# Performance work log

Measured on AMD Instinct MI355X. Metric: run time of the kernel, lower is better.

Reference implementation:

```python
import jax, jax.numpy as jnp
import numpy as np
from jax import lax

COMMITMENT_COST = 0.25

def setup_inputs() -> dict:
    key = jax.random.key(0)
    k1, k2, k3, k4 = jax.random.split(key, 4)
    B, C, H, W, K = 32, 128, 32, 32, 8192
    return {
        "x": jax.random.normal(k1, (B, C, H, W), dtype=jnp.float32),
        "W_lin": jax.random.normal(k2, (C, C), dtype=jnp.float32) * (1.0 / np.sqrt(C)),
        "b_lin": jax.random.normal(k3, (C,), dtype=jnp.float32) * 0.01,
        "emb": jax.random.normal(k4, (K, C), dtype=jnp.float32),
    }

def reference(x, W_lin, b_lin, emb):
    B, C, H, W = x.shape
    K = emb.shape[0]
    # BCHW -> BHWC, then linear projection
    inp = jnp.transpose(x, (0, 2, 3, 1))          # [B,H,W,C]
    inp = inp @ W_lin.T + b_lin                   # nn.Linear
    flat = inp.reshape(-1, C)                     # [N,C], N=B*H*W
    # squared L2 distances to codebook: ||z||^2 + ||e||^2 - 2 z.e
    d = (jnp.sum(flat**2, axis=1, keepdims=True)
         + jnp.sum(emb**2, axis=1)
         - 2.0 * flat @ emb.T)                    # [N,K]
    idx = jnp.argmin(d, axis=1)                   # [N]
    quantized = emb[idx].reshape(inp.shape)       # gather == onehot @ emb
    e_latent = jnp.mean((lax.stop_gradient(quantized) - inp) ** 2)
    q_latent = jnp.mean((quantized - lax.stop_gradient(inp)) ** 2)
    loss = q_latent + COMMITMENT_COST * e_latent
    # straight-through estimator
    quantized_st = inp + lax.stop_gradient(quantized - inp)
    # perplexity from code usage histogram (== mean of one-hot encodings)
    counts = jnp.zeros((K,), dtype=flat.dtype).at[idx].add(1.0)
    avg_probs = counts / flat.shape[0]
    perplexity = jnp.exp(-jnp.sum(avg_probs * jnp.log(avg_probs + 1e-10)))
    out = jnp.transpose(quantized_st, (0, 3, 1, 2))  # back to BCHW
    return (loss, out, perplexity, idx[:, None])
```

## Files before the change

### kernel.cpp

```cpp
#include <hip/hip_runtime.h>
#include <hip/hip_bf16.h>
#include <float.h>

#define NPIX   32768
#define CDIM   128
#define KCB    8192
#define EPS_STOP 0.30f
#define TAUF   0.012f
#define RCAP   8192
#define RCAPA  2048

typedef _Float16 f16x8 __attribute__((ext_vector_type(8)));
typedef float    f32x16 __attribute__((ext_vector_type(16)));

#define WS_EMBFH   0
#define WS_E2      2359296
#define WS_ZWS     2392064
#define WS_CAND    19169280
#define WS_IDX     20217856
#define WS_RLISTA  20348928
#define WS_RLISTB  20381696
#define WS_SCAND   20512768
#define WS_SCANI   21037056
#define WS_COUNTS  21299200
#define WS_LOSS    21331968
#define WS_RCNTA   21331972
#define WS_RCNTB   21331976
#define WS_ZERO_OFF 21299200
#define WS_ZERO_LEN 32780

#define OUT_OFF_OUT  1
#define OUT_OFF_PERP 4194305
#define OUT_OFF_IDX  4194306

__device__ __forceinline__ void ins6(float f, float v[6]) {
    float a = fmaxf(v[0], f); v[0] = fminf(v[0], f);
    float b = fmaxf(v[1], a); v[1] = fminf(v[1], a);
    a = fmaxf(v[2], b); v[2] = fminf(v[2], b);
    b = fmaxf(v[3], a); v[3] = fminf(v[3], a);
    a = fmaxf(v[4], b); v[4] = fminf(v[4], b);
    v[5] = fminf(v[5], a);
}

__global__ __launch_bounds__(256) void k_e2(const float* __restrict__ emb, float* __restrict__ e2) {
    int t = threadIdx.x;
    int wv = t >> 6, l = t & 63;
    int k = blockIdx.x * 4 + wv;
    const float2 v = *(const float2*)&emb[(size_t)k * 128 + l * 2];
    float s = v.x * v.x + v.y * v.y;
    #pragma unroll
    for (int o = 32; o; o >>= 1) s += __shfl_down(s, o, 64);
    if (l == 0) e2[k] = s;
}

__global__ __launch_bounds__(256) void k_prep(const float* __restrict__ emb, const float* __restrict__ e2,
                                              _Float16* __restrict__ embFh) {
    int tid = blockIdx.x * 256 + threadIdx.x;
    int m = tid / 18, r = tid % 18;
    int s = r >> 1, h = r & 1;
    f16x8 hv;
    #pragma unroll
    for (int j = 0; j < 8; ++j) hv[j] = (_Float16)0.0f;
    if (s < 8) {
        int c0 = s * 16 + h * 8;
        const float4 a = *(const float4*)&emb[(size_t)m * 128 + c0];
        const float4 b = *(const float4*)&emb[(size_t)m * 128 + c0 + 4];
        float vals[8] = {a.x, a.y, a.z, a.w, b.x, b.y, b.z, b.w};
        #pragma unroll
        for (int j = 0; j < 8; ++j) hv[j] = (_Float16)(-2.0f * vals[j]);
    } else if (h == 0) {
        float v = e2[m] + 512.0f;
        _Float16 eh = (_Float16)v;
        hv[0] = eh;
        hv[1] = (_Float16)(v - (float)eh);
    }
    size_t base = (((size_t)(m >> 5) * 9 + s) * 64 + (m & 31) + h * 32) * 8;
    *(f16x8*)&embFh[base] = hv;
}

__global__ __launch_bounds__(256, 2) void k_main(
    const float* __restrict__ x, const float* __restrict__ Wl, const float* __restrict__ bl,
    const _Float16* __restrict__ embFh,
    float* __restrict__ zws, float4* __restrict__ cand)
{
    __shared__ __align__(16) float As[64 * 132];
    __shared__ __align__(16) float Xs[64 * 66];
    __shared__ float z2p[256];

    const int t  = threadIdx.x;
    const int n0 = blockIdx.x * 64;
    const int b  = n0 >> 10;
    const int hw0 = n0 & 1023;

    {
        const int p = t & 63, ig = t >> 6;
        float accz[32];
        const float4* bl4 = (const float4*)(bl + ig * 32);
        #pragma unroll
        for (int q = 0; q < 8; ++q) {
            float4 v = bl4[q];
            accz[4*q+0] = v.x; accz[4*q+1] = v.y; accz[4*q+2] = v.z; accz[4*q+3] = v.w;
        }
        for (int hf = 0; hf < 2; ++hf) {
            __syncthreads();
            for (int r = 0; r < 16; ++r) {
                int lin = r * 256 + t;
                int cc = lin >> 6, pp = lin & 63;
                Xs[cc * 66 + pp] = x[(size_t)(b * 128 + hf * 64 + cc) * 1024 + hw0 + pp];
            }
            __syncthreads();
            for (int cc4 = 0; cc4 < 16; ++cc4) {
                float xv0 = Xs[(cc4*4+0) * 66 + p];
                float xv1 = Xs[(cc4*4+1) * 66 + p];
                float xv2 = Xs[(cc4*4+2) * 66 + p];
                float xv3 = Xs[(cc4*4+3) * 66 + p];
                #pragma unroll
                for (int ii = 0; ii < 32; ++ii) {
                    const float4 w4 = *(const float4*)&Wl[(size_t)(ig*32+ii) * 128 + hf*64 + cc4*4];
                    float a = accz[ii];
                    a = fmaf(w4.x, xv0, a);
                    a = fmaf(w4.y, xv1, a);
                    a = fmaf(w4.z, xv2, a);
                    a = fmaf(w4.w, xv3, a);
                    accz[ii] = a;
                }
            }
        }
        float ssq = 0.f;
        float4* ao = (float4*)&As[p * 132 + ig * 32];
        float4* zo = (float4*)(zws + (size_t)(n0 + p) * 128 + ig * 32);
        #pragma unroll
        for (int q = 0; q < 8; ++q) {
            float4 v = make_float4(accz[4*q+0], accz[4*q+1], accz[4*q+2], accz[4*q+3]);
            ao[q] = v;
            zo[q] = v;
            ssq = fmaf(v.x, v.x, fmaf(v.y, v.y, fmaf(v.z, v.z, fmaf(v.w, v.w, ssq))));
        }
        z2p[p * 4 + ig] = ssq;
    }
    __syncthreads();

    const int l = t & 63, w = t >> 6;
    const int half = l >> 5, pcol = l & 31;
    f16x8 B0[9], B1[9];
    #pragma unroll
    for (int nt = 0; nt < 2; ++nt) {
        int p = nt * 32 + pcol;
        #pragma unroll
        for (int s = 0; s < 8; ++s) {
            const float* zp = &As[p * 132 + s * 16 + half * 8];
            float4 v0 = *(const float4*)zp;
            float4 v1 = *(const float4*)(zp + 4);
            float vals[8] = {v0.x, v0.y, v0.z, v0.w, v1.x, v1.y, v1.z, v1.w};
            f16x8 hh;
            #pragma unroll
            for (int j2 = 0; j2 < 8; ++j2) hh[j2] = (_Float16)vals[j2];
            if (nt == 0) B0[s] = hh; else B1[s] = hh;
        }
    }
    {
        f16x8 b8;
        #pragma unroll
        for (int j2 = 0; j2 < 8; ++j2) b8[j2] = (_Float16)0.0f;
        if (half == 0) { b8[0] = (_Float16)1.0f; b8[1] = (_Float16)1.0f; }
        B0[8] = b8; B1[8] = b8;
    }

    auto tree16 = [](const f32x16& v) -> float {
        float a = fminf(fminf(v[0], v[1]), fminf(v[2], v[3]));
        float bb = fminf(fminf(v[4], v[5]), fminf(v[6], v[7]));
        float c = fminf(fminf(v[8], v[9]), fminf(v[10], v[11]));
        float d = fminf(fminf(v[12], v[13]), fminf(v[14], v[15]));
        return fminf(fminf(a, bb), fminf(c, d));
    };

    float gv[6] = {3e38f, 3e38f, 3e38f, 3e38f, 3e38f, 3e38f};
    float hv[6] = {3e38f, 3e38f, 3e38f, 3e38f, 3e38f, 3e38f};
    const f16x8* Ahp = (const f16x8*)embFh;
    f16x8 aE[9], aO[9];
    {
        const f16x8* P = Ahp + (size_t)w * 576 + l;
        #pragma unroll
        for (int s = 0; s < 9; ++s) aE[s] = P[s * 64];
    }
    {
        const f16x8* P = Ahp + (size_t)(w + 4) * 576 + l;
        #pragma unroll
        for (int s = 0; s < 9; ++s) aO[s] = P[s * 64];
    }
    uint32_t idv = (uint32_t)((w << 1) | half);

    for (int g = w; g < 256; g += 8) {
        {
            f32x16 c00 = {}, c01 = {}, c10 = {}, c11 = {};
            #pragma unroll
            for (int s = 0; s < 9; ++s) {
                if (s & 1) {
                    c01 = __builtin_amdgcn_mfma_f32_32x32x16_f16(aE[s], B0[s], c01, 0, 0, 0);
                    c11 = __builtin_amdgcn_mfma_f32_32x32x16_f16(aE[s], B1[s], c11, 0, 0, 0);
                } else {
                    c00 = __builtin_amdgcn_mfma_f32_32x32x16_f16(aE[s], B0[s], c00, 0, 0, 0);
                    c10 = __builtin_amdgcn_mfma_f32_32x32x16_f16(aE[s], B1[s], c10, 0, 0, 0);
                }
            }
            f32x16 s0, s1;
            #pragma unroll
            for (int r = 0; r < 16; ++r) { s0[r] = c00[r] + c01[r]; s1[r] = c10[r] + c11[r]; }
            float m0 = tree16(s0), m1 = tree16(s1);
            ins6(__uint_as_float((__float_as_uint(m0) & 0xFFFFFE00u) | idv), gv);
            ins6(__uint_as_float((__float_as_uint(m1) & 0xFFFFFE00u) | idv), hv);
        }
        {
            int gn = (g + 8 < 256) ? (g + 8) : w;
            const f16x8* P = Ahp + (size_t)gn * 576 + l;
            #pragma unroll
            for (int s = 0; s < 9; ++s) aE[s] = P[s * 64];
        }
        {
            f32x16 c00 = {}, c01 = {}, c10 = {}, c11 = {};
            #pragma unroll
            for (int s = 0; s < 9; ++s) {
                if (s & 1) {
                    c01 = __builtin_amdgcn_mfma_f32_32x32x16_f16(aO[s], B0[s], c01, 0, 0, 0);
                    c11 = __builtin_amdgcn_mfma_f32_32x32x16_f16(aO[s], B1[s], c11, 0, 0, 0);
                } else {
                    c00 = __builtin_amdgcn_mfma_f32_32x32x16_f16(aO[s], B0[s], c00, 0, 0, 0);
                    c10 = __builtin_amdgcn_mfma_f32_32x32x16_f16(aO[s], B1[s], c10, 0, 0, 0);
                }
            }
            f32x16 s0, s1;
            #pragma unroll
            for (int r = 0; r < 16; ++r) { s0[r] = c00[r] + c01[r]; s1[r] = c10[r] + c11[r]; }
            float m0 = tree16(s0), m1 = tree16(s1);
            uint32_t ido = idv + 8u;
            ins6(__uint_as_float((__float_as_uint(m0) & 0xFFFFFE00u) | ido), gv);
            ins6(__uint_as_float((__float_as_uint(m1) & 0xFFFFFE00u) | ido), hv);
        }
        {
            int gn = (g + 12 < 256) ? (g + 12) : w;
            const f16x8* P = Ahp + (size_t)gn * 576 + l;
            #pragma unroll
            for (int s = 0; s < 9; ++s) aO[s] = P[s * 64];
        }
        idv += 16u;
    }

    __syncthreads();
    float* Ms = Xs;
    const int slot = (w << 1) | half;
    #pragma unroll
    for (int q = 0; q < 6; ++q) {
        Ms[(pcol * 8 + slot) * 6 + q] = gv[q];
        Ms[((32 + pcol) * 8 + slot) * 6 + q] = hv[q];
    }
    __syncthreads();
    if (t < 64) {
        float v6[6] = {3e38f, 3e38f, 3e38f, 3e38f, 3e38f, 3e38f};
        #pragma unroll
        for (int s = 0; s < 48; ++s) ins6(Ms[t * 48 + s], v6);
        float z2 = z2p[t*4+0] + z2p[t*4+1] + z2p[t*4+2] + z2p[t*4+3];
        cand[(size_t)(n0 + t) * 2 + 0] = make_float4(v6[0], v6[1], v6[2], v6[3]);
        cand[(size_t)(n0 + t) * 2 + 1] = make_float4(v6[4], v6[5], z2, 0.f);
    }
}

__global__ __launch_bounds__(256) void k_rec(
    const float* __restrict__ zws, const float* __restrict__ emb,
    const float4* __restrict__ cand, int* __restrict__ idxws,
    float* __restrict__ out_idxf, float* __restrict__ losssum,
    int* __restrict__ rlistA, int* __restrict__ rcntA,
    int* __restrict__ rlistB, int* __restrict__ rcntB)
{
    __shared__ float lred[16];
    const int t = threadIdx.x;
    const int pl = t >> 4, j = t & 15;
    const int n = blockIdx.x * 16 + pl;

    const float4 za = *(const float4*)&zws[(size_t)n * 128 + j * 8];
    const float4 zb = *(const float4*)&zws[(size_t)n * 128 + j * 8 + 4];
    const float4 c0 = cand[(size_t)n * 2 + 0];
    const float4 c1 = cand[(size_t)n * 2 + 1];
    const float pv[6] = {c0.x, c0.y, c0.z, c0.w, c1.x, c1.y};
    const float pbase = c1.z - 512.0f;

    float d1 = 3e38f, d2 = 3e38f; int i1 = 0x7fffffff, i2 = 0x7fffffff;
    bool safe = false;
    float lastgmin = 0.f;
    for (int q = 0; q < 6; ++q) {
        uint32_t bits = __float_as_uint(pv[q]);
        float gmin = __uint_as_float(bits & 0xFFFFFE00u);
        lastgmin = gmin;
        if (gmin >= d1 - pbase + EPS_STOP) { safe = true; break; }
        const int mbase = (int)((bits >> 1) & 255u) * 32 + (int)((bits & 1u) << 2);
        #pragma unroll
        for (int c = 0; c < 16; ++c) {
            int m = mbase + (c & 3) + 8 * (c >> 2);
            const float4 ea = *(const float4*)&emb[(size_t)m * 128 + j * 8];
            const float4 eb = *(const float4*)&emb[(size_t)m * 128 + j * 8 + 4];
            float da0 = za.x - ea.x, da1 = za.y - ea.y, da2 = za.z - ea.z, da3 = za.w - ea.w;
            float db0 = zb.x - eb.x, db1 = zb.y - eb.y, db2 = zb.z - eb.z, db3 = zb.w - eb.w;
            float s = da0*da0; s = fmaf(da1, da1, s); s = fmaf(da2, da2, s); s = fmaf(da3, da3, s);
            s = fmaf(db0, db0, s); s = fmaf(db1, db1, s); s = fmaf(db2, db2, s); s = fmaf(db3, db3, s);
            s += __shfl_xor(s, 1, 16);
            s += __shfl_xor(s, 2, 16);
            s += __shfl_xor(s, 4, 16);
            s += __shfl_xor(s, 8, 16);
            if (s < d1 || (s == d1 && m < i1)) { d2 = d1; i2 = i1; d1 = s; i1 = m; }
            else if (s < d2) { d2 = s; i2 = m; }
        }
    }
    if (!safe && lastgmin >= d1 - pbase + EPS_STOP) safe = true;

    if (j == 0) {
        idxws[n] = i1;
        out_idxf[n] = (float)i1;
        if (!safe) {
            int s = atomicAdd(rcntA, 1);
            if (s < RCAPA) rlistA[s] = n;
        } else if ((d2 - d1) < TAUF) {
            int s = atomicAdd(rcntB, 1);
            if (s < RCAP) { int4 v4 = make_int4(n, i1, i2, 0); ((int4*)rlistB)[s] = v4; }
        }
        lred[pl] = d1;
    }
    __syncthreads();
    if (t == 0) {
        float ls = 0.f;
        #pragma unroll
        for (int q = 0; q < 16; ++q) ls += lred[q];
        atomicAdd(losssum, ls);
    }
}

__global__ __launch_bounds__(256) void k_scanp(
    const float* __restrict__ zws, const float* __restrict__ emb,
    const int* __restrict__ rcntA, const int* __restrict__ rlistA,
    double* __restrict__ scand, int* __restrict__ scani)
{
    int cnt = *rcntA; if (cnt > RCAPA) cnt = RCAPA;
    const int t = threadIdx.x;
    const int chunk = blockIdx.x & 31;
    const int gi = t >> 4, j = t & 15;
    __shared__ double sd[16];
    __shared__ int si[16];
    for (int e = blockIdx.x >> 5; e < cnt; e += 64) {
        const int n = rlistA[e];
        const float4 za = *(const float4*)&zws[(size_t)n * 128 + j * 8];
        const float4 zb = *(const float4*)&zws[(size_t)n * 128 + j * 8 + 4];
        double best = 1e300; int bi = 0x7fffffff;
        const int kbase = chunk * 256 + gi * 16;
        for (int c = 0; c < 16; ++c) {
            const int m = kbase + c;
            const float4 ea = *(const float4*)&emb[(size_t)m * 128 + j * 8];
            const float4 eb = *(const float4*)&emb[(size_t)m * 128 + j * 8 + 4];
            double s = 0.0, d;
            d = (double)za.x - (double)ea.x; s += d * d;
            d = (double)za.y - (double)ea.y; s += d * d;
            d = (double)za.z - (double)ea.z; s += d * d;
            d = (double)za.w - (double)ea.w; s += d * d;
            d = (double)zb.x - (double)eb.x; s += d * d;
            d = (double)zb.y - (double)eb.y; s += d * d;
            d = (double)zb.z - (double)eb.z; s += d * d;
            d = (double)zb.w - (double)eb.w; s += d * d;
            s += __shfl_xor(s, 1, 16);
            s += __shfl_xor(s, 2, 16);
            s += __shfl_xor(s, 4, 16);
            s += __shfl_xor(s, 8, 16);
            if (s < best) { best = s; bi = m; }
        }
        __syncthreads();
        if (j == 0) { sd[gi] = best; si[gi] = bi; }
        __syncthreads();
        if (t == 0) {
            double b = sd[0]; int ib = si[0];
            #pragma unroll
            for (int q = 1; q < 16; ++q)
                if (sd[q] < b || (sd[q] == b && si[q] < ib)) { b = sd[q]; ib = si[q]; }
            scand[e * 32 + chunk] = b;
            scani[e * 32 + chunk] = ib;
        }
    }
}

__global__ __launch_bounds__(64) void k_mergeA(
    const int* __restrict__ rcntA, const int* __restrict__ rlistA,
    const double* __restrict__ scand, const int* __restrict__ scani,
    int* __restrict__ idxws, float* __restrict__ out_idxf)
{
    int cnt = *rcntA; if (cnt > RCAPA) cnt = RCAPA;
    const int t = threadIdx.x;
    for (int e = blockIdx.x; e < cnt; e += gridDim.x) {
        double b = 1e300; int ib = 0x7fffffff;
        if (t < 32) { b = scand[e * 32 + t]; ib = scani[e * 32 + t]; }
        #pragma unroll
        for (int o = 16; o; o >>= 1) {
            double ob = __shfl_down(b, o, 64);
            int oi = __shfl_down(ib, o, 64);
            if (ob < b || (ob == b && oi < ib)) { b = ob; ib = oi; }
        }
        if (t == 0) { int n = rlistA[e]; idxws[n] = ib; out_idxf[n] = (float)ib; }
    }
}

__global__ __launch_bounds__(128) void k_pairB(
    const float* __restrict__ x, const float* __restrict__ Wl, const float* __restrict__ bl,
    const float* __restrict__ emb, const int* __restrict__ rcntB, const int* __restrict__ rlistB,
    int* __restrict__ idxws, float* __restrict__ out_idxf)
{
    __shared__ double xs[128];
    __shared__ double red[128];
    int cnt = *rcntB; if (cnt > RCAP) cnt = RCAP;
    const int t = threadIdx.x;
    for (int e = blockIdx.x; e < cnt; e += gridDim.x) {
        const int4 v = ((const int4*)rlistB)[e];
        const int n = v.x, c1 = v.y, c2 = v.z;
        const int b = n >> 10, hw = n & 1023;
        __syncthreads();
        xs[t] = (double)x[(size_t)(b * 128 + t) * 1024 + hw];
        __syncthreads();
        double z = (double)bl[t];
        for (int c = 0; c < 128; ++c) z = fma((double)Wl[(size_t)t * 128 + c], xs[c], z);
        double d1v, d2v;
        double da = z - (double)emb[(size_t)c1 * 128 + t];
        red[t] = da * da; __syncthreads();
        for (int o = 64; o; o >>= 1) { if (t < o) red[t] += red[t + o]; __syncthreads(); }
        d1v = red[0]; __syncthreads();
        double db = z - (double)emb[(size_t)c2 * 128 + t];
        red[t] = db * db; __syncthreads();
        for (int o = 64; o; o >>= 1) { if (t < o) red[t] += red[t + o]; __syncthreads(); }
        d2v = red[0];
        if (t == 0) {
            int win = (d2v < d1v || (d2v == d1v && c2 < c1)) ? c2 : c1;
            idxws[n] = win;
            out_idxf[n] = (float)win;
        }
        __syncthreads();
    }
}

__global__ __launch_bounds__(256) void k_out(
    const float* __restrict__ emb, const int* __restrict__ idxws,
    float* __restrict__ outp , float* __restrict__ counts)
{
    const int t = threadIdx.x;
    const int b = blockIdx.x >> 2, h0 = (blockIdx.x & 3) << 3;
    const int n = b * 1024 + h0 * 32 + t;
    const int id = idxws[n];
    atomicAdd(&counts[id], 1.0f);
    const float4* ep = (const float4*)&emb[(size_t)id * 128];
    float* ob = outp + (size_t)b * 131072 + h0 * 32 + t;
    #pragma unroll 4
    for (int c4 = 0; c4 < 32; ++c4) {
        float4 v = ep[c4];
        ob[(c4 * 4 + 0) * 1024] = v.x;
        ob[(c4 * 4 + 1) * 1024] = v.y;
        ob[(c4 * 4 + 2) * 1024] = v.z;
        ob[(c4 * 4 + 3) * 1024] = v.w;
    }
}

__global__ __launch_bounds__(256) void k_final(
    const float* __restrict__ counts, const float* __restrict__ losssum, float* __restrict__ d_out)
{
    const int t = threadIdx.x;
    float ent = 0.f;
    for (int k = t; k < KCB; k += 256) {
        float p = counts[k] * (1.0f / 32768.0f);
        ent -= p * logf(p + 1e-10f);
    }
    #pragma unroll
    for (int o = 32; o; o >>= 1) ent += __shfl_down(ent, o, 64);
    __shared__ float wred[4];
    if ((t & 63) == 0) wred[t >> 6] = ent;
    __syncthreads();
    if (t == 0) {
        float e = wred[0] + wred[1] + wred[2] + wred[3];
        d_out[0] = 1.25f * (*losssum) * (1.0f / 4194304.0f);
        d_out[OUT_OFF_PERP] = expf(e);
    }
}

extern "C" void kernel_launch(void* const* d_in, const int* in_sizes, int n_in,
                              void* d_out, int out_size, void* d_ws, size_t ws_size,
                              hipStream_t stream) {
    (void)in_sizes; (void)n_in; (void)out_size; (void)ws_size;
    const float* x   = (const float*)d_in[0];
    const float* Wl  = (const float*)d_in[1];
    const float* bl  = (const float*)d_in[2];
    const float* emb = (const float*)d_in[3];
    float* out = (float*)d_out;
    char*  ws  = (char*)d_ws;

    _Float16* embFh = (_Float16*)(ws + WS_EMBFH);
    float* e2      = (float*)(ws + WS_E2);
    float* zws     = (float*)(ws + WS_ZWS);
    float4* cand   = (float4*)(ws + WS_CAND);
    int*   idxws   = (int*)  (ws + WS_IDX);
    int*   rlistA  = (int*)  (ws + WS_RLISTA);
    int*   rlistB  = (int*)  (ws + WS_RLISTB);
    double* scand  = (double*)(ws + WS_SCAND);
    int*   scani   = (int*)  (ws + WS_SCANI);
    float* counts  = (float*)(ws + WS_COUNTS);
    float* losssum = (float*)(ws + WS_LOSS);
    int*   rcntA   = (int*)  (ws + WS_RCNTA);
    int*   rcntB   = (int*)  (ws + WS_RCNTB);

    hipMemsetAsync(ws + WS_ZERO_OFF, 0, WS_ZERO_LEN, stream);

    k_e2<<<KCB / 4, 256, 0, stream>>>(emb, e2);
    k_prep<<<576, 256, 0, stream>>>(emb, e2, embFh);
    k_main<<<NPIX / 64, 256, 0, stream>>>(x, Wl, bl, embFh, zws, cand);
    k_rec<<<NPIX / 16, 256, 0, stream>>>(zws, emb, cand, idxws, out + OUT_OFF_IDX,
                                         losssum, rlistA, rcntA, rlistB, rcntB);
    k_scanp<<<2048, 256, 0, stream>>>(zws, emb, rcntA, rlistA, scand, scani);
    k_mergeA<<<32, 64, 0, stream>>>(rcntA, rlistA, scand, scani, idxws, out + OUT_OFF_IDX);
    k_pairB<<<256, 128, 0, stream>>>(x, Wl, bl, emb, rcntB, rlistB, idxws, out + OUT_OFF_IDX);
    k_out<<<128, 256, 0, stream>>>(emb, idxws, out + OUT_OFF_OUT, counts);
    k_final<<<1, 256, 0, stream>>>(counts, losssum, out);
}
```

Before: 309.6 us.

## Split codebook scan across two blocks per pixel tile and merge candidate lists

k_main now launches twice as many blocks. Each block handles half of the codebook groups for a 64-pixel tile, the tile's projection is recomputed in both blocks, and only the first one writes z. The inner loop is rewritten to a single accumulator pair with interleaved prefetch, and the occupancy hint is raised to 3 blocks per CU. k_rec merges the two 6-candidate lists with a bitonic network before the exact rescoring, and uses a combined tail bound for the safety test. In exchange, the linear projection is computed twice per tile and the candidate buffer doubles in size.

```diff
diff --git a/kernel.cpp b/kernel.cpp
--- a/kernel.cpp
+++ b/kernel.cpp
@@ -17,16 +17,16 @@
 #define WS_E2      2359296
 #define WS_ZWS     2392064
 #define WS_CAND    19169280
-#define WS_IDX     20217856
-#define WS_RLISTA  20348928
-#define WS_RLISTB  20381696
-#define WS_SCAND   20512768
-#define WS_SCANI   21037056
-#define WS_COUNTS  21299200
-#define WS_LOSS    21331968
-#define WS_RCNTA   21331972
-#define WS_RCNTB   21331976
-#define WS_ZERO_OFF 21299200
+#define WS_IDX     21266432
+#define WS_RLISTA  21397504
+#define WS_RLISTB  21430272
+#define WS_SCAND   21561344
+#define WS_SCANI   22085632
+#define WS_COUNTS  22347776
+#define WS_LOSS    22380544
+#define WS_RCNTA   22380548
+#define WS_RCNTB   22380552
+#define WS_ZERO_OFF 22347776
 #define WS_ZERO_LEN 32780
 
 #define OUT_OFF_OUT  1
@@ -78,7 +78,7 @@
     *(f16x8*)&embFh[base] = hv;
 }
 
-__global__ __launch_bounds__(256, 2) void k_main(
+__global__ __launch_bounds__(256, 3) void k_main(
     const float* __restrict__ x, const float* __restrict__ Wl, const float* __restrict__ bl,
     const _Float16* __restrict__ embFh,
     float* __restrict__ zws, float4* __restrict__ cand)
@@ -88,7 +88,9 @@
     __shared__ float z2p[256];
 
     const int t  = threadIdx.x;
-    const int n0 = blockIdx.x * 64;
+    const int pb = blockIdx.x >> 1;
+    const int kh = blockIdx.x & 1;
+    const int n0 = pb * 64;
     const int b  = n0 >> 10;
     const int hw0 = n0 & 1023;
 
@@ -133,7 +135,7 @@
         for (int q = 0; q < 8; ++q) {
             float4 v = make_float4(accz[4*q+0], accz[4*q+1], accz[4*q+2], accz[4*q+3]);
             ao[q] = v;
-            zo[q] = v;
+            if (kh == 0) zo[q] = v;
             ssq = fmaf(v.x, v.x, fmaf(v.y, v.y, fmaf(v.z, v.z, fmaf(v.w, v.w, ssq))));
         }
         z2p[p * 4 + ig] = ssq;
@@ -142,7 +144,7 @@
 
     const int l = t & 63, w = t >> 6;
     const int half = l >> 5, pcol = l & 31;
-    f16x8 B0[9], B1[9];
+    f16x8 B0[8], B1[8], b8;
     #pragma unroll
     for (int nt = 0; nt < 2; ++nt) {
         int p = nt * 32 + pcol;
@@ -159,11 +161,9 @@
         }
     }
     {
-        f16x8 b8;
         #pragma unroll
         for (int j2 = 0; j2 < 8; ++j2) b8[j2] = (_Float16)0.0f;
         if (half == 0) { b8[0] = (_Float16)1.0f; b8[1] = (_Float16)1.0f; }
-        B0[8] = b8; B1[8] = b8;
     }
 
     auto tree16 = [](const f32x16& v) -> float {
@@ -177,72 +177,32 @@
     float gv[6] = {3e38f, 3e38f, 3e38f, 3e38f, 3e38f, 3e38f};
     float hv[6] = {3e38f, 3e38f, 3e38f, 3e38f, 3e38f, 3e38f};
     const f16x8* Ahp = (const f16x8*)embFh;
-    f16x8 aE[9], aO[9];
+    const int g0 = kh * 128 + w;
+    f16x8 a[9];
     {
-        const f16x8* P = Ahp + (size_t)w * 576 + l;
-        #pragma unroll
-        for (int s = 0; s < 9; ++s) aE[s] = P[s * 64];
-    }
-    {
-        const f16x8* P = Ahp + (size_t)(w + 4) * 576 + l;
-        #pragma unroll
-        for (int s = 0; s < 9; ++s) aO[s] = P[s * 64];
-    }
-    uint32_t idv = (uint32_t)((w << 1) | half);
-
-    for (int g = w; g < 256; g += 8) {
-        {
-            f32x16 c00 = {}, c01 = {}, c10 = {}, c11 = {};
-            #pragma unroll
-            for (int s = 0; s < 9; ++s) {
-                if (s & 1) {
-                    c01 = __builtin_amdgcn_mfma_f32_32x32x16_f16(aE[s], B0[s], c01, 0, 0, 0);
-                    c11 = __builtin_amdgcn_mfma_f32_32x32x16_f16(aE[s], B1[s], c11, 0, 0, 0);
-                } else {
-                    c00 = __builtin_amdgcn_mfma_f32_32x32x16_f16(aE[s], B0[s], c00, 0, 0, 0);
-                    c10 = __builtin_amdgcn_mfma_f32_32x32x16_f16(aE[s], B1[s], c10, 0, 0, 0);
-                }
-            }
-            f32x16 s0, s1;
-            #pragma unroll
-            for (int r = 0; r < 16; ++r) { s0[r] = c00[r] + c01[r]; s1[r] = c10[r] + c11[r]; }
-            float m0 = tree16(s0), m1 = tree16(s1);
-            ins6(__uint_as_float((__float_as_uint(m0) & 0xFFFFFE00u) | idv), gv);
-            ins6(__uint_as_float((__float_as_uint(m1) & 0xFFFFFE00u) | idv), hv);
-        }
-        {
-            int gn = (g + 8 < 256) ? (g + 8) : w;
-            const f16x8* P = Ahp + (size_t)gn * 576 + l;
-            #pragma unroll
-            for (int s = 0; s < 9; ++s) aE[s] = P[s * 64];
-        }
-        {
-            f32x16 c00 = {}, c01 = {}, c10 = {}, c11 = {};
-            #pragma unroll
-            for (int s = 0; s < 9; ++s) {
-                if (s & 1) {
-                    c01 = __builtin_amdgcn_mfma_f32_32x32x16_f16(aO[s], B0[s], c01, 0, 0, 0);
-                    c11 = __builtin_amdgcn_mfma_f32_32x32x16_f16(aO[s], B1[s], c11, 0, 0, 0);
-                } else {
-                    c00 = __builtin_amdgcn_mfma_f32_32x32x16_f16(aO[s], B0[s], c00, 0, 0, 0);
-                    c10 = __builtin_amdgcn_mfma_f32_32x32x16_f16(aO[s], B1[s], c10, 0, 0, 0);
-                }
-            }
-            f32x16 s0, s1;
-            #pragma unroll
-            for (int r = 0; r < 16; ++r) { s0[r] = c00[r] + c01[r]; s1[r] = c10[r] + c11[r]; }
-            float m0 = tree16(s0), m1 = tree16(s1);
-            uint32_t ido = idv + 8u;
-            ins6(__uint_as_float((__float_as_uint(m0) & 0xFFFFFE00u) | ido), gv);
-            ins6(__uint_as_float((__float_as_uint(m1) & 0xFFFFFE00u) | ido), hv);
-        }
-        {
-            int gn = (g + 12 < 256) ? (g + 12) : w;
-            const f16x8* P = Ahp + (size_t)gn * 576 + l;
-            #pragma unroll
-            for (int s = 0; s < 9; ++s) aO[s] = P[s * 64];
-        }
-        idv += 16u;
+        const f16x8* P = Ahp + (size_t)g0 * 576 + l;
+        #pragma unroll
+        for (int s = 0; s < 9; ++s) a[s] = P[s * 64];
+    }
+
+    for (int i = 0; i < 32; ++i) {
+        const int g = g0 + i * 4;
+        const int gn = (i < 31) ? (g + 4) : g0;
+        const f16x8* Pn = Ahp + (size_t)gn * 576 + l;
+        f32x16 c0 = {}, c1 = {};
+        #pragma unroll
+        for (int s = 0; s < 8; ++s) {
+            c0 = __builtin_amdgcn_mfma_f32_32x32x16_f16(a[s], B0[s], c0, 0, 0, 0);
+            c1 = __builtin_amdgcn_mfma_f32_32x32x16_f16(a[s], B1[s], c1, 0, 0, 0);
+            a[s] = Pn[s * 64];
+        }
+        c0 = __builtin_amdgcn_mfma_f32_32x32x16_f16(a[8], b8, c0, 0, 0, 0);
+        c1 = __builtin_amdgcn_mfma_f32_32x32x16_f16(a[8], b8, c1, 0, 0, 0);
+        a[8] = Pn[8 * 64];
+        float m0 = tree16(c0), m1 = tree16(c1);
+        const uint32_t id = ((uint32_t)g << 1) | (uint32_t)half;
+        ins6(__uint_as_float((__float_as_uint(m0) & 0xFFFFFE00u) | id), gv);
+        ins6(__uint_as_float((__float_as_uint(m1) & 0xFFFFFE00u) | id), hv);
     }
 
     __syncthreads();
@@ -259,8 +219,9 @@
         #pragma unroll
         for (int s = 0; s < 48; ++s) ins6(Ms[t * 48 + s], v6);
         float z2 = z2p[t*4+0] + z2p[t*4+1] + z2p[t*4+2] + z2p[t*4+3];
-        cand[(size_t)(n0 + t) * 2 + 0] = make_float4(v6[0], v6[1], v6[2], v6[3]);
-        cand[(size_t)(n0 + t) * 2 + 1] = make_float4(v6[4], v6[5], z2, 0.f);
+        size_t cb = (size_t)(n0 + t) * 4 + kh * 2;
+        cand[cb + 0] = make_float4(v6[0], v6[1], v6[2], v6[3]);
+        cand[cb + 1] = make_float4(v6[4], v6[5], kh == 0 ? z2 : 0.f, 0.f);
     }
 }
 
@@ -272,24 +233,44 @@
     int* __restrict__ rlistB, int* __restrict__ rcntB)
 {
     __shared__ float lred[16];
+    __shared__ float vm[16][12];
     const int t = threadIdx.x;
     const int pl = t >> 4, j = t & 15;
     const int n = blockIdx.x * 16 + pl;
 
     const float4 za = *(const float4*)&zws[(size_t)n * 128 + j * 8];
     const float4 zb = *(const float4*)&zws[(size_t)n * 128 + j * 8 + 4];
-    const float4 c0 = cand[(size_t)n * 2 + 0];
-    const float4 c1 = cand[(size_t)n * 2 + 1];
-    const float pv[6] = {c0.x, c0.y, c0.z, c0.w, c1.x, c1.y};
+    const float4 c0 = cand[(size_t)n * 4 + 0];
+    const float4 c1 = cand[(size_t)n * 4 + 1];
+    const float4 c2 = cand[(size_t)n * 4 + 2];
+    const float4 c3 = cand[(size_t)n * 4 + 3];
     const float pbase = c1.z - 512.0f;
+
+    float v[16];
+    v[0] = c0.x; v[1] = c0.y; v[2] = c0.z; v[3] = c0.w; v[4] = c1.x; v[5] = c1.y;
+    v[6] = 3e38f; v[7] = 3e38f;
+    v[8] = 3e38f; v[9] = 3e38f; v[10] = c3.y; v[11] = c3.x;
+    v[12] = c2.w; v[13] = c2.z; v[14] = c2.y; v[15] = c2.x;
+    #define CE(i, k2) { float lo = fminf(v[i], v[k2]); float hi = fmaxf(v[i], v[k2]); v[i] = lo; v[k2] = hi; }
+    CE(0,8) CE(1,9) CE(2,10) CE(3,11) CE(4,12) CE(5,13) CE(6,14) CE(7,15)
+    CE(0,4) CE(1,5) CE(2,6) CE(3,7) CE(8,12) CE(9,13) CE(10,14) CE(11,15)
+    CE(0,2) CE(1,3) CE(4,6) CE(5,7) CE(8,10) CE(9,11) CE(12,14) CE(13,15)
+    CE(0,1) CE(2,3) CE(4,5) CE(6,7) CE(8,9) CE(10,11) CE(12,13) CE(14,15)
+    #undef CE
+    if (j == 0) {
+        vm[pl][0] = v[0]; vm[pl][1] = v[1]; vm[pl][2] = v[2]; vm[pl][3] = v[3];
+        vm[pl][4] = v[4]; vm[pl][5] = v[5]; vm[pl][6] = v[6]; vm[pl][7] = v[7];
+        vm[pl][8] = v[8]; vm[pl][9] = v[9]; vm[pl][10] = v[10]; vm[pl][11] = v[11];
+    }
+    const float tailbound = fminf(__uint_as_float(__float_as_uint(c1.y) & 0xFFFFFE00u),
+                                  __uint_as_float(__float_as_uint(c3.y) & 0xFFFFFE00u));
 
     float d1 = 3e38f, d2 = 3e38f; int i1 = 0x7fffffff, i2 = 0x7fffffff;
     bool safe = false;
-    float lastgmin = 0.f;
-    for (int q = 0; q < 6; ++q) {
-        uint32_t bits = __float_as_uint(pv[q]);
+    for (int q = 0; q < 12; ++q) {
+        float pvq = vm[pl][q];
+        uint32_t bits = __float_as_uint(pvq);
         float gmin = __uint_as_float(bits & 0xFFFFFE00u);
-        lastgmin = gmin;
         if (gmin >= d1 - pbase + EPS_STOP) { safe = true; break; }
         const int mbase = (int)((bits >> 1) & 255u) * 32 + (int)((bits & 1u) << 2);
         #pragma unroll
@@ -309,7 +290,7 @@
             else if (s < d2) { d2 = s; i2 = m; }
         }
     }
-    if (!safe && lastgmin >= d1 - pbase + EPS_STOP) safe = true;
+    if (!safe && tailbound >= d1 - pbase + EPS_STOP) safe = true;
 
     if (j == 0) {
         idxws[n] = i1;
@@ -509,7 +490,7 @@
 
     k_e2<<<KCB / 4, 256, 0, stream>>>(emb, e2);
     k_prep<<<576, 256, 0, stream>>>(emb, e2, embFh);
-    k_main<<<NPIX / 64, 256, 0, stream>>>(x, Wl, bl, embFh, zws, cand);
+    k_main<<<NPIX / 32, 256, 0, stream>>>(x, Wl, bl, embFh, zws, cand);
     k_rec<<<NPIX / 16, 256, 0, stream>>>(zws, emb, cand, idxws, out + OUT_OFF_IDX,
                                          losssum, rlistA, rcntA, rlistB, rcntB);
     k_scanp<<<2048, 256, 0, stream>>>(zws, emb, rcntA, rlistA, scand, scani);
```

Measured after the change: 379.5 us. +22.6%, slower.
